# Kernel tuning notes

Hardware: AMD Instinct MI355X
Metric: run time of the kernel (lower is better)

## Reference

```python
import jax, jax.numpy as jnp
import numpy as np

PAD = 0

def setup_inputs() -> dict:
    key = jax.random.key(0)
    ks = jax.random.split(key, 16)
    B, S, D, F = 64, 512, 768, 256
    VOCAB = 32000
    # variable-length tweets: length in [8, S], rest is padding (token id PAD=0)
    lengths = jax.random.randint(ks[0], (B,), 8, S + 1)
    tok = jax.random.randint(ks[1], (B, S), 1, VOCAB)
    x = jnp.where(jnp.arange(S)[None, :] < lengths[:, None], tok, PAD)
    h = jax.random.normal(ks[2], (B, S, D), dtype=jnp.float32)
    sc = 0.02
    w2 = jax.random.normal(ks[3], (F, D, 2), dtype=jnp.float32) * sc
    b2 = jax.random.normal(ks[4], (F,), dtype=jnp.float32) * sc
    w3 = jax.random.normal(ks[5], (F, D, 3), dtype=jnp.float32) * sc
    b3 = jax.random.normal(ks[6], (F,), dtype=jnp.float32) * sc
    w4 = jax.random.normal(ks[7], (F, D, 4), dtype=jnp.float32) * sc
    b4 = jax.random.normal(ks[8], (F,), dtype=jnp.float32) * sc
    w5 = jax.random.normal(ks[9], (F, D, 5), dtype=jnp.float32) * sc
    b5 = jax.random.normal(ks[10], (F,), dtype=jnp.float32) * sc
    fc_w = jax.random.normal(ks[11], (1, 4 * F), dtype=jnp.float32) * sc
    fc_b = jax.random.normal(ks[12], (1,), dtype=jnp.float32) * sc
    return {"x": x, "h": h, "w2": w2, "b2": b2, "w3": w3, "b3": b3,
            "w4": w4, "b4": b4, "w5": w5, "b5": b5, "fc_w": fc_w, "fc_b": fc_b}


def _branch(hc, L, w, b):
    # hc: [B, D, S] front-compacted hidden states; w: [F, D, k]
    k = w.shape[-1]
    out = jax.lax.conv_general_dilated(
        hc, w, window_strides=(1,), padding='VALID',
        dimension_numbers=('NCH', 'OIH', 'NCH')) + b[None, :, None]  # [B,F,S-k+1]
    T = out.shape[-1]
    # conv position t is valid iff t + k - 1 < L  <=>  t < L - k + 1
    valid = jnp.arange(T)[None, :] < (L - k + 1)[:, None]           # [B,T]
    neg = jnp.asarray(-jnp.inf, out.dtype)
    pooled = jnp.max(jnp.where(valid[:, None, :], out, neg), axis=-1)  # [B,F]
    return jax.nn.relu(pooled)


def reference(x, h, w2, b2, w3, b3, w4, b4, w5, b5, fc_w, fc_b):
    mask = x != PAD                                   # [B,S]
    L = mask.sum(axis=1)                              # [B]
    # stable compaction: move non-pad token hidden states to the front, order preserved
    order = jnp.argsort(jnp.logical_not(mask), axis=1, stable=True)   # [B,S]
    hc = jnp.take_along_axis(h, order[..., None], axis=1)             # [B,S,D]
    hc = hc.transpose(0, 2, 1)                                        # [B,D,S]
    feats = jnp.concatenate([
        _branch(hc, L, w2, b2),
        _branch(hc, L, w3, b3),
        _branch(hc, L, w4, b4),
        _branch(hc, L, w5, b5),
    ], axis=-1)                                       # [B, 4F]
    logits = feats @ fc_w.T + fc_b                    # [B,1]
    return jax.nn.sigmoid(logits).squeeze(-1)         # [B]
```

## Files before the change

### kernel.cpp

```cpp
#include <hip/hip_runtime.h>
#include <stdint.h>

#define Bn 64
#define Sn 512
#define SPn 520
#define Dn 768
#define JSTRIDE 196608
#define ABUF 16640
#define BSLOT 8192
#define QS_A 28.222222f
#define SAQ 0.035433072f

typedef int iv4 __attribute__((ext_vector_type(4)));

static __device__ __forceinline__ signed char q8(float f, float s) {
  float t = __builtin_rintf(f * s);
  t = fmaxf(-127.f, fminf(127.f, t));
  return (signed char)(int)t;
}

static __device__ __forceinline__ void gload16(const void* g, void* l) {
  __builtin_amdgcn_global_load_lds(
      (const __attribute__((address_space(1))) unsigned int*)g,
      (__attribute__((address_space(3))) unsigned int*)l, 16, 0, 0);
}

__global__ __launch_bounds__(256) void stage_kernel(
    const int* __restrict__ x, const float* __restrict__ h,
    const float* __restrict__ w2, const float* __restrict__ w3,
    const float* __restrict__ w4, const float* __restrict__ w5,
    signed char* __restrict__ hcq, signed char* __restrict__ wq,
    float* __restrict__ fscale, int* __restrict__ Lout) {
  int tid = threadIdx.x, lane = tid & 63, wv = tid >> 6;
  if (blockIdx.x < 512) {
    int cidx = blockIdx.x;
    int b = cidx >> 3, rblk = cidx & 7;
    __shared__ unsigned long long masks[8];
    __shared__ short sidx[Sn];
    for (int c = wv; c < 8; c += 4) {
      unsigned long long m = __ballot(x[b * Sn + c * 64 + lane] != 0);
      if (lane == 0) masks[c] = m;
    }
    __syncthreads();
    int pref[9]; pref[0] = 0;
    #pragma unroll
    for (int c = 0; c < 8; ++c) pref[c + 1] = pref[c] + __popcll(masks[c]);
    int L = pref[8];
    if (rblk == 0 && tid == 0) Lout[b] = L;
    for (int p = tid; p < Sn; p += 256) {
      int c = p >> 6, l = p & 63;
      unsigned long long m = masks[c];
      if ((m >> l) & 1ull)
        sidx[pref[c] + __popcll(m & ((1ull << l) - 1ull))] = (short)p;
    }
    __syncthreads();
    int r0 = rblk * 65;
    for (int r = r0 + wv; r < r0 + 65; r += 4) {
      if (r < L) {
        signed char* dst = hcq + ((size_t)b * SPn + r) * Dn;
        const float* src = h + ((size_t)b * Sn + sidx[r]) * Dn;
        #pragma unroll
        for (int c = 0; c < 3; ++c) {
          int d = c * 256 + lane * 4;
          float4 v = *(const float4*)(src + d);
          char4 o = { q8(v.x, QS_A), q8(v.y, QS_A), q8(v.z, QS_A), q8(v.w, QS_A) };
          *(char4*)(dst + d) = o;
        }
      }
    }
  } else {
    __shared__ float sf[3840];
    __shared__ float smax[4];
    int bb = blockIdx.x - 512;
    int br = bb >> 8, f = bb & 255, k = br + 2;
    const float* w = (br == 0) ? w2 : (br == 1) ? w3 : (br == 2) ? w4 : w5;
    int mBase = 256 * ((br * (br + 3)) >> 1);
    const float* src = w + (size_t)f * Dn * k;
    int n = Dn * k;
    float mx = 0.f;
    for (int e = tid; e < n; e += 256) {
      float v = src[e];
      sf[e] = v;
      mx = fmaxf(mx, fabsf(v));
    }
    #pragma unroll
    for (int off = 32; off; off >>= 1) mx = fmaxf(mx, __shfl_xor(mx, off));
    if (lane == 0) smax[wv] = mx;
    __syncthreads();
    float M = fmaxf(fmaxf(smax[0], smax[1]), fmaxf(smax[2], smax[3]));
    M = fmaxf(M, 1e-30f);
    if (tid == 0) fscale[br * 256 + f] = M / 127.f;
    float qs = 127.f / M;
    for (int j = 0; j < k; ++j) {
      signed char* dst = wq + (size_t)(mBase + j * 256 + f) * Dn;
      for (int d4 = tid * 4; d4 < Dn; d4 += 1024) {
        char4 o = { q8(sf[(d4 + 0) * k + j], qs), q8(sf[(d4 + 1) * k + j], qs),
                    q8(sf[(d4 + 2) * k + j], qs), q8(sf[(d4 + 3) * k + j], qs) };
        *(char4*)(dst + d4) = o;
      }
    }
  }
}

__global__ __launch_bounds__(256) void fill_kernel(
    const int* __restrict__ Lbuf, int* __restrict__ plan,
    int* __restrict__ rowmap) {
  __shared__ int sOff[65];
  __shared__ int sL[64];
  int tid = threadIdx.x;
  if (tid < 64) {
    int L = Lbuf[tid];
    int SL = (L + 15) & ~15;
    int pre = SL;
    #pragma unroll
    for (int off = 1; off < 64; off <<= 1) {
      int y = __shfl_up(pre, off);
      if (tid >= off) pre += y;
    }
    sOff[tid] = pre - SL;
    sL[tid] = L;
    if (tid == 63) sOff[64] = pre;
  }
  __syncthreads();
  int b = blockIdx.x;
  int off = sOff[b], L = sL[b];
  int SL = (L + 15) & ~15;
  int enc = (b << 20) | (L << 10);
  for (int t = tid; t < SL; t += 256) rowmap[off + t] = enc | t;
  if (b == 0) {
    int M = sOff[64];
    if (tid == 0) plan[0] = (M + 255) >> 8;
    for (int p = M + tid; p < M + 264; p += 256)
      rowmap[p] = 512;
  }
}

static __device__ __forceinline__ void issueA(
    int d0i, char* sA, const char* const (&gA)[2], const char* gAt,
    int lane, int wvoff) {
  int aoff = (d0i + 1) * 64;
  char* nA = sA + ((d0i + 1) & 1) * ABUF;
  gload16(gA[0] + aoff, nA + wvoff);
  gload16(gA[1] + aoff, nA + 8192 + wvoff);
  if (lane < 16) gload16(gAt + aoff, nA + 16384);
}

template<int KK>
static __device__ __forceinline__ void stageB(
    int d0, char* sB, const char* gB0, int wvoff) {
  int doff = d0 * 64;
  #pragma unroll
  for (int tap = 0; tap < KK; ++tap)
    gload16(gB0 + tap * JSTRIDE + doff, sB + tap * BSLOT + wvoff);
}

template<int KK>
static __device__ __forceinline__ void computeD0(
    int d0, const char* sA, const char* sB, int wr, int wc, int lrow, int lg,
    iv4 (&acc)[4][4]) {
  const char* curA = sA + (d0 & 1) * ABUF;
  #pragma unroll
  for (int j = 0; j < KK; ++j) {
    const char* curB = sB + j * BSLOT;
    iv4 Af[4], Bf[4];
    #pragma unroll
    for (int n = 0; n < 4; ++n) {
      int row = wc * 64 + n * 16 + lrow;
      Bf[n] = *(const iv4*)(curB + row * 64 + ((lg ^ ((row >> 1) & 3)) << 4));
    }
    #pragma unroll
    for (int m = 0; m < 4; ++m) {
      int row = wr * 64 + m * 16 + lrow + j;
      Af[m] = *(const iv4*)(curA + row * 64 + ((lg ^ ((row >> 1) & 3)) << 4));
    }
    __builtin_amdgcn_s_setprio(1);
    #pragma unroll
    for (int n = 0; n < 4; ++n)
      #pragma unroll
      for (int m = 0; m < 4; ++m)
        acc[m][n] = __builtin_amdgcn_mfma_i32_16x16x64_i8(Af[m], Bf[n], acc[m][n], 0, 0, 0);
    __builtin_amdgcn_s_setprio(0);
  }
}

template<int KK>
static __device__ __forceinline__ void conv_loop(
    char* sA, char* sB, const char* const (&gA)[2], const char* gAt,
    const char* gB0, int lane, int wr, int wc, int lrow, int lg, int wvoff,
    iv4 (&acc)[4][4]) {
  gload16(gA[0], sA + wvoff);
  gload16(gA[1], sA + 8192 + wvoff);
  if (lane < 16) gload16(gAt, sA + 16384);
  stageB<KK>(0, sB, gB0, wvoff);
  __syncthreads();
  for (int d0 = 0; d0 < 12; ++d0) {
    if (d0 < 11) issueA(d0, sA, gA, gAt, lane, wvoff);
    computeD0<KK>(d0, sA, sB, wr, wc, lrow, lg, acc);
    __syncthreads();
    if (d0 < 11) {
      stageB<KK>(d0 + 1, sB, gB0, wvoff);
      __syncthreads();
    }
  }
}

__global__ __launch_bounds__(512, 4) void conv_kernel(
    const signed char* __restrict__ hcq, const signed char* __restrict__ wq,
    const float* __restrict__ b2, const float* __restrict__ b3,
    const float* __restrict__ b4, const float* __restrict__ b5,
    const float* __restrict__ fscale,
    const int* __restrict__ plan, const int* __restrict__ rowmap,
    int* __restrict__ feats) {
  __shared__ char smem[2 * ABUF + 5 * BSLOT];
  char* sA = smem;
  char* sB = smem + 2 * ABUF;
  int idx = blockIdx.x;
  int xcd = idx & 7, s2 = idx >> 3;
  int sub = s2 & 7, tile = xcd + ((s2 >> 3) << 3);
  if (tile >= plan[0]) return;
  int br = 3 - (sub >> 1), ff = sub & 1, kk = br + 2;
  int mBase = 256 * ((br * (br + 3)) >> 1) + ff * 128;
  const float* bias = (br == 0) ? b2 : (br == 1) ? b3 : (br == 2) ? b4 : b5;
  int tid = threadIdx.x, lane = tid & 63, wv = tid >> 6;
  int wr = wv >> 1, wc = wv & 1;
  int lrow = lane & 15, lg = lane >> 4;
  int wvoff = wv * 1024;
  int P0 = tile << 8;

  const char* gA[2];
  #pragma unroll
  for (int p = 0; p < 2; ++p) {
    int c = p * 512 + tid;
    int row = c >> 2, sgp = c & 3;
    int rm = rowmap[P0 + row];
    int bb_ = rm >> 20, t = rm & 1023;
    int seg = sgp ^ ((row >> 1) & 3);
    gA[p] = (const char*)(hcq + ((size_t)(bb_ * SPn + t)) * Dn + seg * 16);
  }
  const char* gAt;
  {
    int l = lane & 15;
    int row = 256 + (l >> 2), sgp = l & 3;
    int rm = rowmap[P0 + row];
    int bb_ = rm >> 20, t = rm & 1023;
    int seg = sgp ^ ((row >> 1) & 3);
    gAt = (const char*)(hcq + ((size_t)(bb_ * SPn + t)) * Dn + seg * 16);
  }
  const char* gB0;
  {
    int row = tid >> 2, sgp = tid & 3;
    int seg = sgp ^ ((row >> 1) & 3);
    gB0 = (const char*)(wq + ((size_t)(mBase + row)) * Dn + seg * 16);
  }

  iv4 acc[4][4];
  #pragma unroll
  for (int m = 0; m < 4; ++m)
    #pragma unroll
    for (int n = 0; n < 4; ++n) acc[m][n] = (iv4)0;

  switch (br) {
    case 3: conv_loop<5>(sA, sB, gA, gAt, gB0, lane, wr, wc, lrow, lg, wvoff, acc); break;
    case 2: conv_loop<4>(sA, sB, gA, gAt, gB0, lane, wr, wc, lrow, lg, wvoff, acc); break;
    case 1: conv_loop<3>(sA, sB, gA, gAt, gB0, lane, wr, wc, lrow, lg, wvoff, acc); break;
    default: conv_loop<2>(sA, sB, gA, gAt, gB0, lane, wr, wc, lrow, lg, wvoff, acc); break;
  }

  int rmv[4];
  #pragma unroll
  for (int m = 0; m < 4; ++m) rmv[m] = rowmap[P0 + wr * 64 + m * 16];
  #pragma unroll
  for (int n = 0; n < 4; ++n) {
    int fg = ff * 128 + wc * 64 + n * 16 + lrow;
    float bv = bias[fg];
    float sfc = fscale[br * 256 + fg] * SAQ;
    #pragma unroll
    for (int m = 0; m < 4; ++m) {
      int bb_ = rmv[m] >> 20;
      int Lb = (rmv[m] >> 10) & 1023;
      int t0 = (rmv[m] & 1023) + lg * 4;
      int vlim = Lb - kk + 1;
      float pmax = 0.f;
      #pragma unroll
      for (int i = 0; i < 4; ++i) {
        float v = (float)acc[m][n][i] * sfc + bv;
        pmax = fmaxf(pmax, (t0 + i < vlim) ? fmaxf(v, 0.f) : 0.f);
      }
      pmax = fmaxf(pmax, __shfl_xor(pmax, 16));
      pmax = fmaxf(pmax, __shfl_xor(pmax, 32));
      if (lane < 16 && pmax > 0.f)
        atomicMax(feats + bb_ * 1024 + br * 256 + fg, __float_as_int(pmax));
    }
  }
}

__global__ __launch_bounds__(64) void fc_kernel(
    const int* __restrict__ feats, const float* __restrict__ fcw,
    const float* __restrict__ fcb, float* __restrict__ out) {
  int b = blockIdx.x, lane = threadIdx.x;
  float acc = 0.f;
  for (int i = lane; i < 1024; i += 64)
    acc += __int_as_float(feats[b * 1024 + i]) * fcw[i];
  #pragma unroll
  for (int off = 32; off; off >>= 1) acc += __shfl_xor(acc, off);
  if (lane == 0) out[b] = 1.f / (1.f + expf(-(acc + fcb[0])));
}

extern "C" void kernel_launch(void* const* d_in, const int* in_sizes, int n_in,
                              void* d_out, int out_size, void* d_ws, size_t ws_size,
                              hipStream_t stream) {
  const int*   x   = (const int*)d_in[0];
  const float* h   = (const float*)d_in[1];
  const float* w2  = (const float*)d_in[2];
  const float* b2  = (const float*)d_in[3];
  const float* w3  = (const float*)d_in[4];
  const float* b3  = (const float*)d_in[5];
  const float* w4  = (const float*)d_in[6];
  const float* b4  = (const float*)d_in[7];
  const float* w5  = (const float*)d_in[8];
  const float* b5  = (const float*)d_in[9];
  const float* fcw = (const float*)d_in[10];
  const float* fcb = (const float*)d_in[11];
  float* out = (float*)d_out;
  char* ws = (char*)d_ws;
  signed char* hcq = (signed char*)ws;
  signed char* wq  = (signed char*)(ws + 25559040);
  float* fscale = (float*)(ws + 28311552);
  int* feats  = (int*)(ws + 28315648);
  int* Lbuf   = (int*)(ws + 28577792);
  int* plan   = (int*)(ws + 28578048);
  int* rowmap = (int*)(ws + 28578064);

  hipMemsetAsync(feats, 0, 64 * 1024 * 4, stream);
  stage_kernel<<<1536, 256, 0, stream>>>(x, h, w2, w3, w4, w5, hcq, wq, fscale, Lbuf);
  fill_kernel<<<64, 256, 0, stream>>>(Lbuf, plan, rowmap);
  conv_kernel<<<1024, 512, 0, stream>>>(hcq, wq, b2, b3, b4, b5, fscale, plan, rowmap, feats);
  fc_kernel<<<64, 64, 0, stream>>>(feats, fcw, fcb, out);
}
```

Before: 106.7 us.

## Load conv weights directly into registers and fold feats zeroing into fill kernel

The conv kernel stops staging int8 weight tiles through LDS. Each wave now loads its B fragments for all taps straight from global memory into registers per depth step, which drops the second __syncthreads per iteration and shrinks shared memory to the A double buffer. The memset of feats is removed and the zeroing is done inside fill_kernel, saving one launch. The launch_bounds minimum-blocks hint is also dropped. In exchange, register pressure rises (up to 20 iv4 B fragments held at once), weight loads become uncoalesced per-lane global reads that rely on cache hits, and occupancy may fall.

```diff
diff --git a/kernel.cpp b/kernel.cpp
--- a/kernel.cpp
+++ b/kernel.cpp
@@ -7,7 +7,6 @@
 #define Dn 768
 #define JSTRIDE 196608
 #define ABUF 16640
-#define BSLOT 8192
 #define QS_A 28.222222f
 #define SAQ 0.035433072f
 
@@ -104,10 +103,15 @@
 
 __global__ __launch_bounds__(256) void fill_kernel(
     const int* __restrict__ Lbuf, int* __restrict__ plan,
-    int* __restrict__ rowmap) {
+    int* __restrict__ rowmap, int* __restrict__ feats) {
   __shared__ int sOff[65];
   __shared__ int sL[64];
   int tid = threadIdx.x;
+  int b = blockIdx.x;
+  {
+    int4 z = {0, 0, 0, 0};
+    *(int4*)(feats + b * 1024 + tid * 4) = z;
+  }
   if (tid < 64) {
     int L = Lbuf[tid];
     int SL = (L + 15) & ~15;
@@ -122,7 +126,6 @@
     if (tid == 63) sOff[64] = pre;
   }
   __syncthreads();
-  int b = blockIdx.x;
   int off = sOff[b], L = sL[b];
   int SL = (L + 15) & ~15;
   int enc = (b << 20) | (L << 10);
@@ -135,6 +138,36 @@
   }
 }
 
+template<int KK>
+static __device__ __forceinline__ void computeD0(
+    int d0, const char* sA, const char* const (&gB)[4],
+    int wr, int lrow, int lg, iv4 (&acc)[4][4]) {
+  int doff = d0 * 64;
+  iv4 Bv[5][4];
+  #pragma unroll
+  for (int j = 0; j < KK; ++j)
+    #pragma unroll
+    for (int n = 0; n < 4; ++n)
+      Bv[j][n] = *(const iv4*)(gB[n] + j * JSTRIDE + doff);
+  const char* curA = sA + (d0 & 1) * ABUF;
+  #pragma unroll
+  for (int j = 0; j < KK; ++j) {
+    iv4 Af[4];
+    #pragma unroll
+    for (int m = 0; m < 4; ++m) {
+      int row = wr * 64 + m * 16 + lrow + j;
+      Af[m] = *(const iv4*)(curA + row * 64 + ((lg ^ ((row >> 1) & 3)) << 4));
+    }
+    __builtin_amdgcn_s_setprio(1);
+    #pragma unroll
+    for (int n = 0; n < 4; ++n)
+      #pragma unroll
+      for (int m = 0; m < 4; ++m)
+        acc[m][n] = __builtin_amdgcn_mfma_i32_16x16x64_i8(Af[m], Bv[j][n], acc[m][n], 0, 0, 0);
+    __builtin_amdgcn_s_setprio(0);
+  }
+}
+
 static __device__ __forceinline__ void issueA(
     int d0i, char* sA, const char* const (&gA)[2], const char* gAt,
     int lane, int wvoff) {
@@ -146,74 +179,31 @@
 }
 
 template<int KK>
-static __device__ __forceinline__ void stageB(
-    int d0, char* sB, const char* gB0, int wvoff) {
-  int doff = d0 * 64;
-  #pragma unroll
-  for (int tap = 0; tap < KK; ++tap)
-    gload16(gB0 + tap * JSTRIDE + doff, sB + tap * BSLOT + wvoff);
-}
-
-template<int KK>
-static __device__ __forceinline__ void computeD0(
-    int d0, const char* sA, const char* sB, int wr, int wc, int lrow, int lg,
-    iv4 (&acc)[4][4]) {
-  const char* curA = sA + (d0 & 1) * ABUF;
-  #pragma unroll
-  for (int j = 0; j < KK; ++j) {
-    const char* curB = sB + j * BSLOT;
-    iv4 Af[4], Bf[4];
-    #pragma unroll
-    for (int n = 0; n < 4; ++n) {
-      int row = wc * 64 + n * 16 + lrow;
-      Bf[n] = *(const iv4*)(curB + row * 64 + ((lg ^ ((row >> 1) & 3)) << 4));
-    }
-    #pragma unroll
-    for (int m = 0; m < 4; ++m) {
-      int row = wr * 64 + m * 16 + lrow + j;
-      Af[m] = *(const iv4*)(curA + row * 64 + ((lg ^ ((row >> 1) & 3)) << 4));
-    }
-    __builtin_amdgcn_s_setprio(1);
-    #pragma unroll
-    for (int n = 0; n < 4; ++n)
-      #pragma unroll
-      for (int m = 0; m < 4; ++m)
-        acc[m][n] = __builtin_amdgcn_mfma_i32_16x16x64_i8(Af[m], Bf[n], acc[m][n], 0, 0, 0);
-    __builtin_amdgcn_s_setprio(0);
-  }
-}
-
-template<int KK>
 static __device__ __forceinline__ void conv_loop(
-    char* sA, char* sB, const char* const (&gA)[2], const char* gAt,
-    const char* gB0, int lane, int wr, int wc, int lrow, int lg, int wvoff,
-    iv4 (&acc)[4][4]) {
+    char* sA, const char* const (&gA)[2], const char* gAt,
+    const char* const (&gB)[4],
+    int lane, int wr, int lrow, int lg, int wvoff, iv4 (&acc)[4][4]) {
   gload16(gA[0], sA + wvoff);
   gload16(gA[1], sA + 8192 + wvoff);
   if (lane < 16) gload16(gAt, sA + 16384);
-  stageB<KK>(0, sB, gB0, wvoff);
   __syncthreads();
-  for (int d0 = 0; d0 < 12; ++d0) {
-    if (d0 < 11) issueA(d0, sA, gA, gAt, lane, wvoff);
-    computeD0<KK>(d0, sA, sB, wr, wc, lrow, lg, acc);
+  for (int d0 = 0; d0 < 11; ++d0) {
+    issueA(d0, sA, gA, gAt, lane, wvoff);
+    computeD0<KK>(d0, sA, gB, wr, lrow, lg, acc);
     __syncthreads();
-    if (d0 < 11) {
-      stageB<KK>(d0 + 1, sB, gB0, wvoff);
-      __syncthreads();
-    }
-  }
-}
-
-__global__ __launch_bounds__(512, 4) void conv_kernel(
+  }
+  computeD0<KK>(11, sA, gB, wr, lrow, lg, acc);
+}
+
+__global__ __launch_bounds__(512) void conv_kernel(
     const signed char* __restrict__ hcq, const signed char* __restrict__ wq,
     const float* __restrict__ b2, const float* __restrict__ b3,
     const float* __restrict__ b4, const float* __restrict__ b5,
     const float* __restrict__ fscale,
     const int* __restrict__ plan, const int* __restrict__ rowmap,
     int* __restrict__ feats) {
-  __shared__ char smem[2 * ABUF + 5 * BSLOT];
+  __shared__ char smem[2 * ABUF];
   char* sA = smem;
-  char* sB = smem + 2 * ABUF;
   int idx = blockIdx.x;
   int xcd = idx & 7, s2 = idx >> 3;
   int sub = s2 & 7, tile = xcd + ((s2 >> 3) << 3);
@@ -246,12 +236,10 @@
     int seg = sgp ^ ((row >> 1) & 3);
     gAt = (const char*)(hcq + ((size_t)(bb_ * SPn + t)) * Dn + seg * 16);
   }
-  const char* gB0;
-  {
-    int row = tid >> 2, sgp = tid & 3;
-    int seg = sgp ^ ((row >> 1) & 3);
-    gB0 = (const char*)(wq + ((size_t)(mBase + row)) * Dn + seg * 16);
-  }
+  const char* gB[4];
+  #pragma unroll
+  for (int n = 0; n < 4; ++n)
+    gB[n] = (const char*)(wq + (size_t)(mBase + wc * 64 + n * 16 + lrow) * Dn + lg * 16);
 
   iv4 acc[4][4];
   #pragma unroll
@@ -260,10 +248,10 @@
     for (int n = 0; n < 4; ++n) acc[m][n] = (iv4)0;
 
   switch (br) {
-    case 3: conv_loop<5>(sA, sB, gA, gAt, gB0, lane, wr, wc, lrow, lg, wvoff, acc); break;
-    case 2: conv_loop<4>(sA, sB, gA, gAt, gB0, lane, wr, wc, lrow, lg, wvoff, acc); break;
-    case 1: conv_loop<3>(sA, sB, gA, gAt, gB0, lane, wr, wc, lrow, lg, wvoff, acc); break;
-    default: conv_loop<2>(sA, sB, gA, gAt, gB0, lane, wr, wc, lrow, lg, wvoff, acc); break;
+    case 3: conv_loop<5>(sA, gA, gAt, gB, lane, wr, lrow, lg, wvoff, acc); break;
+    case 2: conv_loop<4>(sA, gA, gAt, gB, lane, wr, lrow, lg, wvoff, acc); break;
+    case 1: conv_loop<3>(sA, gA, gAt, gB, lane, wr, lrow, lg, wvoff, acc); break;
+    default: conv_loop<2>(sA, gA, gAt, gB, lane, wr, lrow, lg, wvoff, acc); break;
   }
 
   int rmv[4];
@@ -331,9 +319,8 @@
   int* plan   = (int*)(ws + 28578048);
   int* rowmap = (int*)(ws + 28578064);
 
-  hipMemsetAsync(feats, 0, 64 * 1024 * 4, stream);
   stage_kernel<<<1536, 256, 0, stream>>>(x, h, w2, w3, w4, w5, hcq, wq, fscale, Lbuf);
-  fill_kernel<<<64, 256, 0, stream>>>(Lbuf, plan, rowmap);
+  fill_kernel<<<64, 256, 0, stream>>>(Lbuf, plan, rowmap, feats);
   conv_kernel<<<1024, 512, 0, stream>>>(hcq, wq, b2, b3, b4, b5, fscale, plan, rowmap, feats);
   fc_kernel<<<64, 64, 0, stream>>>(feats, fcw, fcb, out);
 }
```

After: 187.0 us. 75.3% more time.
